# Kernel optimization log

Hardware: AMD Instinct MI355X
Metric: run time of the kernel (lower is better)

## Reference

```python
import jax, jax.numpy as jnp
import numpy as np

SEQ, BATCH, INP = 20, 16384, 2
HID, EMB = 256, 64
TARGET_LEN = 30


def setup_inputs() -> dict:
    key = jax.random.key(0)
    ks = jax.random.split(key, 12)
    s = 0.1
    return {
        "x_input": jax.random.normal(ks[0], (SEQ, BATCH, INP), dtype=jnp.float32),
        # encoder embedding Linear(input_size -> emb_dim)
        "W_emb": jax.random.normal(ks[1], (EMB, INP), dtype=jnp.float32) * s,
        "b_emb": jax.random.normal(ks[2], (EMB,), dtype=jnp.float32) * s,
        # encoder LSTM (input EMB -> hidden HID), PyTorch gate order i,f,g,o; bias = b_ih + b_hh
        "W_ih_enc": jax.random.normal(ks[3], (4 * HID, EMB), dtype=jnp.float32) * s,
        "W_hh_enc": jax.random.normal(ks[4], (4 * HID, HID), dtype=jnp.float32) * s,
        "b_enc": jax.random.normal(ks[5], (4 * HID,), dtype=jnp.float32) * s,
        # decoder LSTM (input INP -> hidden HID)
        "W_ih_dec": jax.random.normal(ks[6], (4 * HID, INP), dtype=jnp.float32) * s,
        "W_hh_dec": jax.random.normal(ks[7], (4 * HID, HID), dtype=jnp.float32) * s,
        "b_dec": jax.random.normal(ks[8], (4 * HID,), dtype=jnp.float32) * s,
        # decoder output Linear(hidden -> input_size)
        "W_out": jax.random.normal(ks[9], (INP, HID), dtype=jnp.float32) * s,
        "b_out": jax.random.normal(ks[10], (INP,), dtype=jnp.float32) * s,
        "target_len": TARGET_LEN,
    }


def _lstm_cell(x, h, c, W_ih, W_hh, b):
    # x: [B, in], h/c: [B, H]; PyTorch gate order: input, forget, cell(g), output
    gates = x @ W_ih.T + h @ W_hh.T + b  # [B, 4H]
    i, f, g, o = jnp.split(gates, 4, axis=-1)
    c_new = jax.nn.sigmoid(f) * c + jax.nn.sigmoid(i) * jnp.tanh(g)
    h_new = jax.nn.sigmoid(o) * jnp.tanh(c_new)
    return h_new, c_new


def reference(x_input, W_emb, b_emb, W_ih_enc, W_hh_enc, b_enc,
              W_ih_dec, W_hh_dec, b_dec, W_out, b_out, target_len):
    B = x_input.shape[1]
    # --- encoder ---
    x_emb = x_input @ W_emb.T + b_emb  # [S, B, EMB]
    h0 = jnp.zeros((B, HID), dtype=x_input.dtype)
    c0 = jnp.zeros((B, HID), dtype=x_input.dtype)

    def enc_step(carry, xt):
        h, c = carry
        h, c = _lstm_cell(xt, h, c, W_ih_enc, W_hh_enc, b_enc)
        return (h, c), None

    (h_enc, c_enc), _ = jax.lax.scan(enc_step, (h0, c0), x_emb)

    dec_in0 = x_input[-1]  # [B, INP]

    def dec_step(carry, _):
        di, h, c = carry
        h, c = _lstm_cell(di, h, c, W_ih_dec, W_hh_dec, b_dec)
        out = h @ W_out.T + b_out  # [B, INP]
        return (out, h, c), out

    _, outputs = jax.lax.scan(dec_step, (dec_in0, h_enc, c_enc), None,
                              length=int(target_len))
    return outputs  # [target_len, B, INP]
```

## Files before the change

kernel.cpp:

```cpp
#include <hip/hip_runtime.h>


#define SEQ  20
#define TLEN 30
#define LOG2E  1.442695041f
#define LOG2E2 2.885390082f

typedef _Float16 half8   __attribute__((ext_vector_type(8)));
typedef _Float16 half4   __attribute__((ext_vector_type(4)));
typedef float    floatx4 __attribute__((ext_vector_type(4)));

__device__ _Float16 g_w_enc[1024 * 288];
__device__ _Float16 g_w_dec0[1024 * 288];
__device__ _Float16 g_w_deff[1024 * 288];
__device__ _Float16 g_wout[512];

__global__ void prep_kernel(const float* __restrict__ W_emb,
                            const float* __restrict__ b_emb,
                            const float* __restrict__ W_ih_enc,
                            const float* __restrict__ W_hh_enc,
                            const float* __restrict__ b_enc,
                            const float* __restrict__ W_ih_dec,
                            const float* __restrict__ W_hh_dec,
                            const float* __restrict__ b_dec,
                            const float* __restrict__ W_out,
                            const float* __restrict__ b_out) {
    int gid = blockIdx.x * blockDim.x + threadIdx.x;
    int stride = gridDim.x * blockDim.x;
    for (int s = gid; s < 1024 * 288; s += stride) {
        int n = s / 288, k = s - n * 288;
        int g = n >> 8, c = (n >> 4) & 15, l16 = n & 15;
        int w = c >> 1, cc = c & 1;
        int i = cc * 4 + g;
        int kt = k >> 5, q = (k >> 3) & 3, j = k & 7;
        int dst = ((w * 9 + kt) * 8 + i) * 512 + q * 128 + l16 * 8 + j;
        float sc = (g == 2) ? LOG2E2 : LOG2E;
        float fe = 0.f, fd = 0.f, ff = 0.f;
        if (k < 256) {
            fe = W_hh_enc[n * 256 + k];
            fd = W_hh_dec[n * 256 + k];
            ff = fd + W_ih_dec[2 * n] * W_out[k]
                    + W_ih_dec[2 * n + 1] * W_out[256 + k];
        } else {
            int kp = k - 256;
            if (kp < 2) {
                fd = W_ih_dec[2 * n + kp];
                const float* wr = &W_ih_enc[n * 64];
                for (int e = 0; e < 64; e++) fe = fmaf(wr[e], W_emb[2 * e + kp], fe);
            } else if (kp == 2) {
                fd = b_dec[n];
                ff = b_dec[n] + W_ih_dec[2 * n] * b_out[0]
                              + W_ih_dec[2 * n + 1] * b_out[1];
                fe = b_enc[n];
                const float* wr = &W_ih_enc[n * 64];
                for (int e = 0; e < 64; e++) fe = fmaf(wr[e], b_emb[e], fe);
            }
        }
        g_w_enc[dst]  = (_Float16)(fe * sc);
        g_w_dec0[dst] = (_Float16)(fd * sc);
        g_w_deff[dst] = (_Float16)(ff * sc);
    }
    if (gid < 512) g_wout[gid] = (_Float16)W_out[gid];
}

__global__ __launch_bounds__(512, 2) void lstm_fused(
        const float* __restrict__ x_input,
        const float* __restrict__ b_out,
        float* __restrict__ out)
{
    __shared__ __align__(16) _Float16 h_pack[2][18432];
    __shared__ __align__(16) float    partial_lds[2][8 * 132];

    const int tid = threadIdx.x;
    const int w   = tid >> 6;
    const int L   = tid & 63;
    const int l16 = L & 15;
    const int q   = L >> 4;
    const long row0 = (long)blockIdx.x * 64;

    {
        int* hz = (int*)&h_pack[0][0];
        for (int idx = tid; idx < 18432; idx += 512) hz[idx] = 0;
    }
    __syncthreads();
    if (tid < 128) {
        int buf = tid >> 6, b = tid & 63;
        h_pack[buf][((b >> 4) * 9 + 8) * 512 + (b & 15) * 8 + 2] = (_Float16)1.f;
    }
    if (tid < 128) {
        int b = tid >> 1, jj = tid & 1;
        h_pack[0][((b >> 4) * 9 + 8) * 512 + (b & 15) * 8 + jj] =
            (_Float16)x_input[(row0 + b) * 2 + jj];
    }

    const float bo = b_out[tid & 1];
    const int aoff = q * 128 + l16 * 8;
    const _Float16* __restrict__ wenc_w  = &g_w_enc[w * 36864];
    const _Float16* __restrict__ wdec0_w = &g_w_dec0[w * 36864];
    const _Float16* __restrict__ wdeff_w = &g_w_deff[w * 36864];

    _Float16 wo[2][2][4];
#pragma unroll
    for (int jj = 0; jj < 2; jj++)
#pragma unroll
        for (int cc = 0; cc < 2; cc++)
#pragma unroll
            for (int r = 0; r < 4; r++)
                wo[jj][cc][r] = g_wout[jj * 256 + 32 * w + 16 * cc + 4 * q + r];

    floatx4 acc[8][4];
    float   c_st[4][2][4];
#pragma unroll
    for (int nt = 0; nt < 4; nt++)
#pragma unroll
        for (int cc = 0; cc < 2; cc++)
#pragma unroll
            for (int r = 0; r < 4; r++) c_st[nt][cc][r] = 0.f;

    __syncthreads();

    int cur = 0;
#pragma unroll 1
    for (int t = 0; t < SEQ + TLEN; t++) {
        const _Float16* __restrict__ Wb =
            (t < SEQ) ? wenc_w : (t == SEQ) ? wdec0_w : wdeff_w;
        const _Float16* __restrict__ hp = h_pack[cur];
        _Float16* __restrict__ hn = h_pack[cur ^ 1];

#pragma unroll
        for (int kt = 0; kt < 9; kt++) {
            half8 B[4];
#pragma unroll
            for (int nt = 0; nt < 4; nt++)
                B[nt] = *(const half8*)&hp[(nt * 9 + kt) * 512 + aoff];
#pragma unroll
            for (int i = 0; i < 8; i++) {
                half8 Aw = *(const half8*)&Wb[(kt * 8 + i) * 512 + aoff];
                if (kt == 0) {
#pragma unroll
                    for (int nt = 0; nt < 4; nt++)
                        acc[i][nt] = __builtin_amdgcn_mfma_f32_16x16x32_f16(
                            Aw, B[nt], (floatx4)(0.f), 0, 0, 0);
                } else {
#pragma unroll
                    for (int nt = 0; nt < 4; nt++)
                        acc[i][nt] = __builtin_amdgcn_mfma_f32_16x16x32_f16(
                            Aw, B[nt], acc[i][nt], 0, 0, 0);
                }
            }
        }

        float xval = 0.f;
        if (t < SEQ && tid < 128) {
            int srct = (t + 1 < SEQ) ? t + 1 : SEQ - 1;
            xval = x_input[(long)srct * 32768 + (row0 + (tid >> 1)) * 2 + (tid & 1)];
        }

        const bool dec = (t >= SEQ);
        float po[4][2];
#pragma unroll
        for (int nt = 0; nt < 4; nt++) { po[nt][0] = 0.f; po[nt][1] = 0.f; }

#pragma unroll
        for (int nt = 0; nt < 4; nt++)
#pragma unroll
            for (int cc = 0; cc < 2; cc++) {
                half4 hv4;
                float hvf[4];
#pragma unroll
                for (int r = 0; r < 4; r++) {
                    float ai = acc[cc * 4 + 0][nt][r];
                    float af = acc[cc * 4 + 1][nt][r];
                    float ag = acc[cc * 4 + 2][nt][r];
                    float ao = acc[cc * 4 + 3][nt][r];
                    float eI = __builtin_amdgcn_exp2f(-ai);
                    float eG = __builtin_amdgcn_exp2f(-ag);
                    float eF = __builtin_amdgcn_exp2f(-af);
                    float eO = __builtin_amdgcn_exp2f(-ao);
                    float ig = (1.f - eG) *
                        __builtin_amdgcn_rcpf((1.f + eI) * (1.f + eG));
                    float fs = __builtin_amdgcn_rcpf(1.f + eF);
                    float cn = fmaf(fs, c_st[nt][cc][r], ig);
                    c_st[nt][cc][r] = cn;
                    float cnc = fminf(fmaxf(cn, -12.f), 12.f);
                    float eC = __builtin_amdgcn_exp2f(-LOG2E2 * cnc);
                    float hv = (1.f - eC) *
                        __builtin_amdgcn_rcpf((1.f + eO) * (1.f + eC));
                    hvf[r] = hv;
                    hv4[r] = (_Float16)hv;
                }
                *(half4*)&hn[(nt * 9 + w) * 512 + (2 * cc + (q >> 1)) * 128 +
                             l16 * 8 + 4 * (q & 1)] = hv4;
                if (dec) {
#pragma unroll
                    for (int r = 0; r < 4; r++) {
                        po[nt][0] = fmaf(hvf[r], (float)wo[0][cc][r], po[nt][0]);
                        po[nt][1] = fmaf(hvf[r], (float)wo[1][cc][r], po[nt][1]);
                    }
                }
            }

        if (dec) {
#pragma unroll
            for (int nt = 0; nt < 4; nt++)
#pragma unroll
                for (int jj = 0; jj < 2; jj++) {
                    float s = po[nt][jj];
                    s += __shfl_xor(s, 16);
                    s += __shfl_xor(s, 32);
                    po[nt][jj] = s;
                }
            if (q == 0) {
                float* pl = &partial_lds[t & 1][w * 132];
#pragma unroll
                for (int nt = 0; nt < 4; nt++) {
                    pl[nt * 16 + l16]      = po[nt][0];
                    pl[66 + nt * 16 + l16] = po[nt][1];
                }
            }
        }

        if (t < SEQ && tid < 128) {
            int b = tid >> 1, jj = tid & 1;
            hn[((b >> 4) * 9 + 8) * 512 + (b & 15) * 8 + jj] = (_Float16)xval;
        }

        __syncthreads();

        if (dec && tid < 128) {
            int m = tid >> 1, jj = tid & 1;
            const float* pl = &partial_lds[t & 1][jj * 66 + m];
            float s = bo;
#pragma unroll
            for (int w8 = 0; w8 < 8; w8++) s += pl[w8 * 132];
            out[(long)(t - SEQ) * 32768 + (row0 + m) * 2 + jj] = s;
        }

        cur ^= 1;
    }
}

extern "C" void kernel_launch(void* const* d_in, const int* in_sizes, int n_in,
                              void* d_out, int out_size, void* d_ws, size_t ws_size,
                              hipStream_t stream) {
    (void)in_sizes; (void)n_in; (void)d_ws; (void)ws_size; (void)out_size;
    const float* x      = (const float*)d_in[0];
    const float* W_emb  = (const float*)d_in[1];
    const float* b_emb  = (const float*)d_in[2];
    const float* W_ih_e = (const float*)d_in[3];
    const float* W_hh_e = (const float*)d_in[4];
    const float* b_enc  = (const float*)d_in[5];
    const float* W_ih_d = (const float*)d_in[6];
    const float* W_hh_d = (const float*)d_in[7];
    const float* b_dec  = (const float*)d_in[8];
    const float* W_out  = (const float*)d_in[9];
    const float* b_out  = (const float*)d_in[10];
    float* outp = (float*)d_out;

    prep_kernel<<<512, 256, 0, stream>>>(W_emb, b_emb, W_ih_e, W_hh_e, b_enc,
                                         W_ih_d, W_hh_d, b_dec, W_out, b_out);
    lstm_fused<<<256, 512, 0, stream>>>(x, b_out, outp);
}
```

Measured before the change: 587.3 us.

## Replace per-step block barrier with per-slice LDS flags and last-wave output reduction

Removes the `__syncthreads` at the end of each timestep. Each wave now publishes a workgroup-scope release flag once it has written its slice of the next hidden state, and consumers spin on that slice's flag just before loading it in the K loop. This lets waves start the next step's MFMAs on ready slices without waiting for the whole block. The decoder output reduction is done by whichever wave arrives last on an atomic counter, and the x input load and store are moved to wave 0 with vectorized accesses. The cost is spin-wait polling with s_sleep, more atomics, and subtle memory-ordering requirements on the double-buffered LDS.

Result: slower. 614.2 us (+4.6%).

```diff
diff --git a/kernel.cpp b/kernel.cpp
--- a/kernel.cpp
+++ b/kernel.cpp
@@ -8,6 +8,7 @@
 
 typedef _Float16 half8   __attribute__((ext_vector_type(8)));
 typedef _Float16 half4   __attribute__((ext_vector_type(4)));
+typedef _Float16 half2v  __attribute__((ext_vector_type(2)));
 typedef float    floatx4 __attribute__((ext_vector_type(4)));
 
 __device__ _Float16 g_w_enc[1024 * 288];
@@ -70,6 +71,8 @@
 {
     __shared__ __align__(16) _Float16 h_pack[2][18432];
     __shared__ __align__(16) float    partial_lds[2][8 * 132];
+    __shared__ int flag_lds[9];
+    __shared__ int cnt_lds[2];
 
     const int tid = threadIdx.x;
     const int w   = tid >> 6;
@@ -81,6 +84,8 @@
     {
         int* hz = (int*)&h_pack[0][0];
         for (int idx = tid; idx < 18432; idx += 512) hz[idx] = 0;
+        if (tid < 9) flag_lds[tid] = 0;
+        if (tid < 2) cnt_lds[tid] = 0;
     }
     __syncthreads();
     if (tid < 128) {
@@ -93,7 +98,7 @@
             (_Float16)x_input[(row0 + b) * 2 + jj];
     }
 
-    const float bo = b_out[tid & 1];
+    const float2 bo2 = make_float2(b_out[0], b_out[1]);
     const int aoff = q * 128 + l16 * 8;
     const _Float16* __restrict__ wenc_w  = &g_w_enc[w * 36864];
     const _Float16* __restrict__ wdec0_w = &g_w_dec0[w * 36864];
@@ -119,16 +124,28 @@
 
     __syncthreads();
 
-    int cur = 0;
+    auto flag_ld = [&](int idx) {
+        return __hip_atomic_load(&flag_lds[idx], __ATOMIC_RELAXED,
+                                 __HIP_MEMORY_SCOPE_WORKGROUP);
+    };
+
 #pragma unroll 1
     for (int t = 0; t < SEQ + TLEN; t++) {
         const _Float16* __restrict__ Wb =
             (t < SEQ) ? wenc_w : (t == SEQ) ? wdec0_w : wdeff_w;
-        const _Float16* __restrict__ hp = h_pack[cur];
-        _Float16* __restrict__ hn = h_pack[cur ^ 1];
-
+        const _Float16* __restrict__ hp = h_pack[t & 1];
+        _Float16* __restrict__ hn = h_pack[(t + 1) & 1];
+
+        int pf = flag_ld(0);
 #pragma unroll
         for (int kt = 0; kt < 9; kt++) {
+            int pfn = 0;
+            if (kt < 8) pfn = flag_ld(kt + 1);
+            while (pf < t) {
+                __builtin_amdgcn_s_sleep(1);
+                pf = flag_ld(kt);
+            }
+            __builtin_amdgcn_sched_barrier(0);
             half8 B[4];
 #pragma unroll
             for (int nt = 0; nt < 4; nt++)
@@ -148,15 +165,17 @@
                             Aw, B[nt], acc[i][nt], 0, 0, 0);
                 }
             }
-        }
-
-        float xval = 0.f;
-        if (t < SEQ && tid < 128) {
+            pf = pfn;
+        }
+
+        float2 xv2 = make_float2(0.f, 0.f);
+        if (w == 0 && t < SEQ) {
             int srct = (t + 1 < SEQ) ? t + 1 : SEQ - 1;
-            xval = x_input[(long)srct * 32768 + (row0 + (tid >> 1)) * 2 + (tid & 1)];
+            xv2 = *(const float2*)&x_input[(long)srct * 32768 + (row0 + L) * 2];
         }
 
         const bool dec = (t >= SEQ);
+        const int par = t & 1;
         float po[4][2];
 #pragma unroll
         for (int nt = 0; nt < 4; nt++) { po[nt][0] = 0.f; po[nt][1] = 0.f; }
@@ -200,6 +219,20 @@
                 }
             }
 
+        if (L == 0)
+            __hip_atomic_store(&flag_lds[w], t + 1, __ATOMIC_RELEASE,
+                               __HIP_MEMORY_SCOPE_WORKGROUP);
+
+        if (w == 0) {
+            if (t < SEQ) {
+                half2v xh; xh[0] = (_Float16)xv2.x; xh[1] = (_Float16)xv2.y;
+                *(half2v*)&hn[((L >> 4) * 9 + 8) * 512 + (L & 15) * 8] = xh;
+            }
+            if (L == 0)
+                __hip_atomic_store(&flag_lds[8], t + 1, __ATOMIC_RELEASE,
+                                   __HIP_MEMORY_SCOPE_WORKGROUP);
+        }
+
         if (dec) {
 #pragma unroll
             for (int nt = 0; nt < 4; nt++)
@@ -211,32 +244,31 @@
                     po[nt][jj] = s;
                 }
             if (q == 0) {
-                float* pl = &partial_lds[t & 1][w * 132];
+                float* pl = &partial_lds[par][w * 132];
 #pragma unroll
                 for (int nt = 0; nt < 4; nt++) {
                     pl[nt * 16 + l16]      = po[nt][0];
                     pl[66 + nt * 16 + l16] = po[nt][1];
                 }
             }
-        }
-
-        if (t < SEQ && tid < 128) {
-            int b = tid >> 1, jj = tid & 1;
-            hn[((b >> 4) * 9 + 8) * 512 + (b & 15) * 8 + jj] = (_Float16)xval;
-        }
-
-        __syncthreads();
-
-        if (dec && tid < 128) {
-            int m = tid >> 1, jj = tid & 1;
-            const float* pl = &partial_lds[t & 1][jj * 66 + m];
-            float s = bo;
-#pragma unroll
-            for (int w8 = 0; w8 < 8; w8++) s += pl[w8 * 132];
-            out[(long)(t - SEQ) * 32768 + (row0 + m) * 2 + jj] = s;
-        }
-
-        cur ^= 1;
+            __threadfence_block();
+            int arr = 0;
+            if (L == 0) arr = atomicAdd(&cnt_lds[par], 1);
+            arr = __shfl(arr, 0);
+            if (arr == 7) {
+                if (L == 0)
+                    __hip_atomic_store(&cnt_lds[par], 0, __ATOMIC_RELAXED,
+                                       __HIP_MEMORY_SCOPE_WORKGROUP);
+                float s0 = bo2.x, s1 = bo2.y;
+#pragma unroll
+                for (int w8 = 0; w8 < 8; w8++) {
+                    s0 += partial_lds[par][w8 * 132 + L];
+                    s1 += partial_lds[par][w8 * 132 + 66 + L];
+                }
+                *(float2*)&out[(long)(t - SEQ) * 32768 + (row0 + L) * 2] =
+                    make_float2(s0, s1);
+            }
+        }
     }
 }
 
```
